# Kernel optimization log

Hardware: AMD Instinct MI355X
Metric: run time of the kernel (lower is better)

The kernel has to match this reference:

```python
import jax, jax.numpy as jnp
import numpy as np

N, E = 20000, 5000
IN_FT, OUT_FT = 128, 128
DENSITY = 0.01  # fraction of nonzeros in the incidence matrix


def setup_inputs() -> dict:
    key = jax.random.key(0)
    kx, kh, kw, kb = jax.random.split(key, 4)
    X = jax.random.normal(kx, (N, IN_FT), dtype=jnp.float32)
    H = (jax.random.uniform(kh, (N, E)) < DENSITY).astype(jnp.float32)
    # xavier_normal_ with gain=0.01
    xav_std = 0.01 * np.sqrt(2.0 / (IN_FT + OUT_FT))
    weight_trans = jax.random.normal(kw, (IN_FT, OUT_FT), dtype=jnp.float32) * xav_std
    bias = jax.random.normal(kb, (OUT_FT,), dtype=jnp.float32) * 0.01
    return {"X": X, "H": H, "weight_trans": weight_trans, "bias": bias}


def reference(X, H, weight_trans, bias):
    # X: [N, in_ft], H: [N, E] incidence
    Xw = X @ weight_trans                      # [N, out_ft]
    DV = jnp.sum(H, axis=1) + 1e-12            # node degrees, [N]
    DE = jnp.sum(H, axis=0) + 1e-12            # hyperedge degrees, [E]
    # G = diag(1/DV) @ H @ diag(1/DE) @ H^T applied to Xw, computed in the
    # efficient order without materializing the NxN matrix G:
    M = H.T @ Xw                               # [E, out_ft]
    M = M / DE[:, None]                        # diag(1/DE) scaling
    out = H @ M                                # [N, out_ft]
    out = out / DV[:, None]                    # diag(1/DV) scaling
    out = out + bias
    return jax.nn.relu(out)
```

## Files before the change

kernel.cpp:

```cpp
#include <hip/hip_runtime.h>
#include <hip/hip_bf16.h>

typedef unsigned long long u64;
typedef __attribute__((ext_vector_type(4))) float f32x4v;

#define N_NODES 20000
#define N_EDGES 5000
#define FT 128
#define NT 20
#define NRG 313
#define ROW_U64 80
#define COL_STRIDE 5120
#define MAX_DEG 320
#define MAX_NDEG 128

#define NTLOAD(p) __builtin_nontemporal_load((const f32x4v*)(p))

__global__ __launch_bounds__(256) void scan_fused(
    const float* __restrict__ H, u64* __restrict__ Hbt, u64* __restrict__ HbtT,
    const float2* __restrict__ X2, __hip_bfloat162* __restrict__ Xb2) {
  const int wid = threadIdx.x >> 6, lane = threadIdx.x & 63;

  if (blockIdx.x >= 1565) {
    for (int i = (blockIdx.x - 1565) * 256 + threadIdx.x; i < 1280000;
         i += 320 * 256)
      Xb2[i] = __float22bfloat162_rn(X2[i]);
    return;
  }

  const int gw = blockIdx.x * 4 + wid;
  const int t = gw % NT, rg = gw / NT;
  const int r0 = rg * 64;
  const int rows = min(64, N_NODES - r0);
  const int idx4 = t * 64 + lane;
  const bool lv = idx4 < 1250;

  u64 m0 = 0, m1 = 0, m2 = 0, m3 = 0;
  for (int kb = 0; kb < rows; kb += 8) {
    f32x4v vv[8];
#pragma unroll
    for (int k = 0; k < 8; ++k) vv[k] = (f32x4v){0.f, 0.f, 0.f, 0.f};
    if (lv) {
      const float* bp = H + (size_t)(r0 + kb) * N_EDGES + idx4 * 4;
#pragma unroll
      for (int k = 0; k < 8; ++k) vv[k] = NTLOAD(bp + (size_t)k * N_EDGES);
    }
#pragma unroll
    for (int k = 0; k < 8; ++k) {
      u64 b0 = __ballot(vv[k].x != 0.f);
      u64 b1 = __ballot(vv[k].y != 0.f);
      u64 b2 = __ballot(vv[k].z != 0.f);
      u64 b3 = __ballot(vv[k].w != 0.f);
      const bool keep = (lane == kb + k);
      m0 = keep ? b0 : m0;  m1 = keep ? b1 : m1;
      m2 = keep ? b2 : m2;  m3 = keep ? b3 : m3;
    }
  }
  if (lane < rows) {
    u64* hp = Hbt + (size_t)(r0 + lane) * ROW_U64 + t * 4;
    hp[0] = m0; hp[1] = m1; hp[2] = m2; hp[3] = m3;
  }
  u64 t0 = 0, t1 = 0, t2 = 0, t3 = 0;
  for (int l = 0; l < 64; ++l) {
    u64 c0 = __ballot((m0 >> l) & 1ull);
    u64 c1 = __ballot((m1 >> l) & 1ull);
    u64 c2 = __ballot((m2 >> l) & 1ull);
    u64 c3 = __ballot((m3 >> l) & 1ull);
    const bool keep = (lane == l);
    t0 = keep ? c0 : t0;  t1 = keep ? c1 : t1;
    t2 = keep ? c2 : t2;  t3 = keep ? c3 : t3;
  }
  u64* op = HbtT + (size_t)rg * COL_STRIDE + t * 256 + 4 * lane;
  op[0] = t0; op[1] = t1; op[2] = t2; op[3] = t3;
}

__global__ __launch_bounds__(256) void edge_gather(
    const __hip_bfloat162* __restrict__ Xb2,
    const u64* __restrict__ HbtT,
    float2* __restrict__ P2, int* __restrict__ de) {
  __shared__ int sidx[4][MAX_DEG];
  const int wid = threadIdx.x >> 6, lane = threadIdx.x & 63;
  const int e = blockIdx.x * 4 + wid;

  u64 cm[5];
#pragma unroll
  for (int q = 0; q < 5; ++q) {
    int u = q * 64 + lane;
    cm[q] = (u < NRG) ? HbtT[(size_t)u * COL_STRIDE + e] : 0ull;
  }
  int cnt = 0;
#pragma unroll
  for (int q = 0; q < 5; ++q) cnt += __popcll(cm[q]);
  int off = cnt;
  for (int d = 1; d < 64; d <<= 1) {
    int v = __shfl_up(off, d);
    if (lane >= d) off += v;
  }
  int total = __shfl(off, 63);
  off -= cnt;
#pragma unroll
  for (int q = 0; q < 5; ++q) {
    u64 w = cm[q];
    int rbase = q * 4096 + lane * 64;
    while (w) {
      int b = __ffsll(w) - 1;
      w &= w - 1;
      if (off < MAX_DEG) sidx[wid][off] = rbase + b;
      ++off;
    }
  }
  __builtin_amdgcn_s_waitcnt(0);
  int tt = min(total, MAX_DEG);

  float sx = 0.f, sy = 0.f;
  int g = 0;
  for (; g + 16 <= tt; g += 16) {
    int nn[16];
#pragma unroll
    for (int q = 0; q < 16; ++q) nn[q] = sidx[wid][g + q];
    float2 aa[16];
#pragma unroll
    for (int q = 0; q < 16; ++q) aa[q] = __bfloat1622float2(Xb2[nn[q] * 64 + lane]);
#pragma unroll
    for (int q = 0; q < 16; ++q) { sx += aa[q].x; sy += aa[q].y; }
  }
  for (; g < tt; ++g) {
    float2 a2 = __bfloat1622float2(Xb2[sidx[wid][g] * 64 + lane]);
    sx += a2.x; sy += a2.y;
  }
  P2[e * 64 + lane] = make_float2(sx, sy);
  if (lane == 0) de[e] = total;
}

__global__ __launch_bounds__(256) void gemm_M(
    const float* __restrict__ P, const float* __restrict__ W,
    const int* __restrict__ de, float* __restrict__ M) {
  int f = threadIdx.x & (FT - 1);
  int half = threadIdx.x >> 7;
  int base = blockIdx.x * 16 + half * 8;
#pragma unroll
  for (int g = 0; g < 8; g += 4) {
    int e = base + g;
    if (e >= N_EDGES) break;
    const float* p0 = P + (e + 0) * FT;
    const float* p1 = P + (e + 1) * FT;
    const float* p2 = P + (e + 2) * FT;
    const float* p3 = P + (e + 3) * FT;
    float a0 = 0.f, a1 = 0.f, a2 = 0.f, a3 = 0.f;
#pragma unroll 4
    for (int k = 0; k < FT; ++k) {
      float w = W[k * FT + f];
      a0 += p0[k] * w; a1 += p1[k] * w; a2 += p2[k] * w; a3 += p3[k] * w;
    }
    M[(e + 0) * FT + f] = a0 / ((float)de[e + 0] + 1e-12f);
    M[(e + 1) * FT + f] = a1 / ((float)de[e + 1] + 1e-12f);
    M[(e + 2) * FT + f] = a2 / ((float)de[e + 2] + 1e-12f);
    M[(e + 3) * FT + f] = a3 / ((float)de[e + 3] + 1e-12f);
  }
}

__global__ __launch_bounds__(256) void row_apply(
    const u64* __restrict__ Hbt,
    const float2* __restrict__ M2, const float2* __restrict__ bias2,
    float2* __restrict__ out2) {
  __shared__ int eidx[4][MAX_NDEG];
  const int wid = threadIdx.x >> 6, lane = threadIdx.x & 63;
  const int n = blockIdx.x * 4 + wid;
  const u64* hp = Hbt + (size_t)n * ROW_U64;
  u64 mlo = hp[lane];
  u64 mhi = (lane < ROW_U64 - 64) ? hp[64 + lane] : 0ull;
  int cnt = __popcll(mlo) + __popcll(mhi);
  int off = cnt;
  for (int d = 1; d < 64; d <<= 1) {
    int v = __shfl_up(off, d);
    if (lane >= d) off += v;
  }
  int total = __shfl(off, 63);
  off -= cnt;
  {
    int eb = (lane >> 2) * 256 + (lane & 3);
    u64 w = mlo;
    while (w) {
      int b = __ffsll(w) - 1; w &= w - 1;
      if (off < MAX_NDEG) eidx[wid][off] = eb + 4 * b;
      ++off;
    }
    int vp = 64 + lane;
    eb = (vp >> 2) * 256 + (vp & 3);
    w = mhi;
    while (w) {
      int b = __ffsll(w) - 1; w &= w - 1;
      if (off < MAX_NDEG) eidx[wid][off] = eb + 4 * b;
      ++off;
    }
  }
  __builtin_amdgcn_s_waitcnt(0);
  int tt = min(total, MAX_NDEG);

  float sx = 0.f, sy = 0.f;
  int g = 0;
  for (; g + 8 <= tt; g += 8) {
    int ee[8];
#pragma unroll
    for (int q = 0; q < 8; ++q) ee[q] = eidx[wid][g + q];
    float2 vv[8];
#pragma unroll
    for (int q = 0; q < 8; ++q) vv[q] = M2[(size_t)ee[q] * 64 + lane];
#pragma unroll
    for (int q = 0; q < 8; ++q) { sx += vv[q].x; sy += vv[q].y; }
  }
  for (; g < tt; ++g) {
    float2 v = M2[(size_t)eidx[wid][g] * 64 + lane];
    sx += v.x; sy += v.y;
  }
  float inv = 1.f / ((float)total + 1e-12f);
  float2 bb = bias2[lane];
  float2 o;
  o.x = fmaxf(fmaf(sx, inv, bb.x), 0.f);
  o.y = fmaxf(fmaf(sy, inv, bb.y), 0.f);
  out2[(size_t)n * 64 + lane] = o;
}

extern "C" void kernel_launch(void* const* d_in, const int* in_sizes, int n_in,
                              void* d_out, int out_size, void* d_ws, size_t ws_size,
                              hipStream_t stream) {
  const float* X    = (const float*)d_in[0];
  const float* H    = (const float*)d_in[1];
  const float* W    = (const float*)d_in[2];
  const float* bias = (const float*)d_in[3];
  float* out = (float*)d_out;

  int* ws = (int*)d_ws;
  u64* Hbt             = (u64*)ws;
  u64* HbtT            = (u64*)(ws + 3200000);
  __hip_bfloat162* Xb2 = (__hip_bfloat162*)(ws + 6476800);
  float* P             = (float*)(ws + 7756800);
  int* de              = ws + 8396800;
  float* M             = (float*)(ws + 8401920);

  scan_fused <<<1885, 256, 0, stream>>>(H, Hbt, HbtT, (const float2*)X, Xb2);
  edge_gather<<<1250, 256, 0, stream>>>(Xb2, HbtT, (float2*)P, de);
  gemm_M     <<<313, 256, 0, stream>>>(P, W, de, M);
  row_apply  <<<5000, 256, 0, stream>>>(Hbt, (const float2*)M,
                                        (const float2*)bias, (float2*)out);
}
```

Baseline: 613.8 us.

## Replace sparse gathers with dense bitmask-expanded MFMA GEMMs over the incidence matrix

Replaces the index-list gather kernels with three bf16 MFMA GEMMs. X@W is computed first, then H^T·Xw and H·M run as dense matmuls whose H operand is built on the fly by expanding bitmask bits into bf16 ones. Hbt is rewritten with interleaved bit packing so node rows map directly to MFMA fragments. This removes irregular gathers and per-wave index compaction, at the cost of doing dense work over a 1%-dense matrix and adding bf16 rounding on Xw and M.

```diff
diff --git a/kernel.cpp b/kernel.cpp
--- a/kernel.cpp
+++ b/kernel.cpp
@@ -2,7 +2,11 @@
 #include <hip/hip_bf16.h>
 
 typedef unsigned long long u64;
+typedef unsigned int u32;
+typedef unsigned short u16;
 typedef __attribute__((ext_vector_type(4))) float f32x4v;
+typedef __attribute__((ext_vector_type(16))) float f32x16;
+typedef __attribute__((ext_vector_type(8))) short bf16x8;
 
 #define N_NODES 20000
 #define N_EDGES 5000
@@ -11,20 +15,49 @@
 #define NRG 313
 #define ROW_U64 80
 #define COL_STRIDE 5120
-#define MAX_DEG 320
-#define MAX_NDEG 128
+#define XWT_S 20032
 
 #define NTLOAD(p) __builtin_nontemporal_load((const f32x4v*)(p))
+
+static __device__ __forceinline__ u64 spread4(u64 x) {
+  x = (x | (x << 24)) & 0x000000FF000000FFull;
+  x = (x | (x << 12)) & 0x000F000F000F000Full;
+  x = (x | (x << 6))  & 0x0303030303030303ull;
+  x = (x | (x << 3))  & 0x1111111111111111ull;
+  return x;
+}
+
+static __device__ __forceinline__ u16 f2bf(float x) {
+  u32 u = __float_as_uint(x);
+  u = (u + 0x7FFFu + ((u >> 16) & 1u)) >> 16;
+  return (u16)u;
+}
+
+static __device__ __forceinline__ bf16x8 expand8(u32 b) {
+  union { u32 u[4]; bf16x8 v; } r;
+  r.u[0] = (( b        & 1u) | ((( b >> 1) & 1u) << 16)) * 0x3F80u;
+  r.u[1] = (((b >> 2)  & 1u) | ((( b >> 3) & 1u) << 16)) * 0x3F80u;
+  r.u[2] = (((b >> 4)  & 1u) | ((( b >> 5) & 1u) << 16)) * 0x3F80u;
+  r.u[3] = (((b >> 6)  & 1u) | ((( b >> 7) & 1u) << 16)) * 0x3F80u;
+  return r.v;
+}
 
 __global__ __launch_bounds__(256) void scan_fused(
     const float* __restrict__ H, u64* __restrict__ Hbt, u64* __restrict__ HbtT,
-    const float2* __restrict__ X2, __hip_bfloat162* __restrict__ Xb2) {
+    const float2* __restrict__ X2, __hip_bfloat162* __restrict__ Xb2,
+    const float* __restrict__ Wf, u16* __restrict__ WtB) {
   const int wid = threadIdx.x >> 6, lane = threadIdx.x & 63;
 
   if (blockIdx.x >= 1565) {
     for (int i = (blockIdx.x - 1565) * 256 + threadIdx.x; i < 1280000;
          i += 320 * 256)
       Xb2[i] = __float22bfloat162_rn(X2[i]);
+    if (blockIdx.x == 1884) {
+      for (int i = threadIdx.x; i < FT * FT; i += 256) {
+        int f = i >> 7, k = i & 127;
+        WtB[i] = f2bf(Wf[k * FT + f]);
+      }
+    }
     return;
   }
 
@@ -58,7 +91,14 @@
   }
   if (lane < rows) {
     u64* hp = Hbt + (size_t)(r0 + lane) * ROW_U64 + t * 4;
-    hp[0] = m0; hp[1] = m1; hp[2] = m2; hp[3] = m3;
+#pragma unroll
+    for (int j = 0; j < 4; ++j) {
+      u64 p = spread4((m0 >> (16 * j)) & 0xFFFFull)
+            | (spread4((m1 >> (16 * j)) & 0xFFFFull) << 1)
+            | (spread4((m2 >> (16 * j)) & 0xFFFFull) << 2)
+            | (spread4((m3 >> (16 * j)) & 0xFFFFull) << 3);
+      hp[j] = p;
+    }
   }
   u64 t0 = 0, t1 = 0, t2 = 0, t3 = 0;
   for (int l = 0; l < 64; ++l) {
@@ -74,151 +114,107 @@
   op[0] = t0; op[1] = t1; op[2] = t2; op[3] = t3;
 }
 
-__global__ __launch_bounds__(256) void edge_gather(
-    const __hip_bfloat162* __restrict__ Xb2,
-    const u64* __restrict__ HbtT,
-    float2* __restrict__ P2, int* __restrict__ de) {
-  __shared__ int sidx[4][MAX_DEG];
-  const int wid = threadIdx.x >> 6, lane = threadIdx.x & 63;
-  const int e = blockIdx.x * 4 + wid;
-
-  u64 cm[5];
-#pragma unroll
-  for (int q = 0; q < 5; ++q) {
-    int u = q * 64 + lane;
-    cm[q] = (u < NRG) ? HbtT[(size_t)u * COL_STRIDE + e] : 0ull;
-  }
-  int cnt = 0;
-#pragma unroll
-  for (int q = 0; q < 5; ++q) cnt += __popcll(cm[q]);
-  int off = cnt;
-  for (int d = 1; d < 64; d <<= 1) {
-    int v = __shfl_up(off, d);
-    if (lane >= d) off += v;
-  }
-  int total = __shfl(off, 63);
-  off -= cnt;
-#pragma unroll
-  for (int q = 0; q < 5; ++q) {
-    u64 w = cm[q];
-    int rbase = q * 4096 + lane * 64;
-    while (w) {
-      int b = __ffsll(w) - 1;
-      w &= w - 1;
-      if (off < MAX_DEG) sidx[wid][off] = rbase + b;
-      ++off;
-    }
-  }
-  __builtin_amdgcn_s_waitcnt(0);
-  int tt = min(total, MAX_DEG);
-
-  float sx = 0.f, sy = 0.f;
-  int g = 0;
-  for (; g + 16 <= tt; g += 16) {
-    int nn[16];
-#pragma unroll
-    for (int q = 0; q < 16; ++q) nn[q] = sidx[wid][g + q];
-    float2 aa[16];
-#pragma unroll
-    for (int q = 0; q < 16; ++q) aa[q] = __bfloat1622float2(Xb2[nn[q] * 64 + lane]);
-#pragma unroll
-    for (int q = 0; q < 16; ++q) { sx += aa[q].x; sy += aa[q].y; }
-  }
-  for (; g < tt; ++g) {
-    float2 a2 = __bfloat1622float2(Xb2[sidx[wid][g] * 64 + lane]);
-    sx += a2.x; sy += a2.y;
-  }
-  P2[e * 64 + lane] = make_float2(sx, sy);
-  if (lane == 0) de[e] = total;
-}
-
-__global__ __launch_bounds__(256) void gemm_M(
-    const float* __restrict__ P, const float* __restrict__ W,
-    const int* __restrict__ de, float* __restrict__ M) {
-  int f = threadIdx.x & (FT - 1);
-  int half = threadIdx.x >> 7;
-  int base = blockIdx.x * 16 + half * 8;
-#pragma unroll
-  for (int g = 0; g < 8; g += 4) {
-    int e = base + g;
-    if (e >= N_EDGES) break;
-    const float* p0 = P + (e + 0) * FT;
-    const float* p1 = P + (e + 1) * FT;
-    const float* p2 = P + (e + 2) * FT;
-    const float* p3 = P + (e + 3) * FT;
-    float a0 = 0.f, a1 = 0.f, a2 = 0.f, a3 = 0.f;
-#pragma unroll 4
-    for (int k = 0; k < FT; ++k) {
-      float w = W[k * FT + f];
-      a0 += p0[k] * w; a1 += p1[k] * w; a2 += p2[k] * w; a3 += p3[k] * w;
-    }
-    M[(e + 0) * FT + f] = a0 / ((float)de[e + 0] + 1e-12f);
-    M[(e + 1) * FT + f] = a1 / ((float)de[e + 1] + 1e-12f);
-    M[(e + 2) * FT + f] = a2 / ((float)de[e + 2] + 1e-12f);
-    M[(e + 3) * FT + f] = a3 / ((float)de[e + 3] + 1e-12f);
-  }
-}
-
-__global__ __launch_bounds__(256) void row_apply(
-    const u64* __restrict__ Hbt,
-    const float2* __restrict__ M2, const float2* __restrict__ bias2,
-    float2* __restrict__ out2) {
-  __shared__ int eidx[4][MAX_NDEG];
-  const int wid = threadIdx.x >> 6, lane = threadIdx.x & 63;
-  const int n = blockIdx.x * 4 + wid;
-  const u64* hp = Hbt + (size_t)n * ROW_U64;
-  u64 mlo = hp[lane];
-  u64 mhi = (lane < ROW_U64 - 64) ? hp[64 + lane] : 0ull;
-  int cnt = __popcll(mlo) + __popcll(mhi);
-  int off = cnt;
-  for (int d = 1; d < 64; d <<= 1) {
-    int v = __shfl_up(off, d);
-    if (lane >= d) off += v;
-  }
-  int total = __shfl(off, 63);
-  off -= cnt;
+__global__ __launch_bounds__(256) void gemm_xw(
+    const u16* __restrict__ Xb, const u16* __restrict__ WtB,
+    u16* __restrict__ XwT) {
+  const int wave = threadIdx.x >> 6, lane = threadIdx.x & 63;
+  const int col = lane & 31, half = lane >> 5;
+  const int n0 = blockIdx.x * 32;
+  const int f0 = wave * 32;
+  if (n0 >= N_NODES) {
+    if (lane < 32)
+      for (int r = 0; r < 32; ++r)
+        XwT[(size_t)(f0 + r) * XWT_S + n0 + lane] = 0;
+    return;
+  }
+  f32x16 acc;
+#pragma unroll
+  for (int i = 0; i < 16; ++i) acc[i] = 0.f;
+  for (int k0 = 0; k0 < FT; k0 += 16) {
+    bf16x8 a = *(const bf16x8*)(WtB + (f0 + col) * FT + k0 + half * 8);
+    bf16x8 b = *(const bf16x8*)(Xb + (size_t)(n0 + col) * FT + k0 + half * 8);
+    acc = __builtin_amdgcn_mfma_f32_32x32x16_bf16(a, b, acc, 0, 0, 0);
+  }
+#pragma unroll
+  for (int r = 0; r < 16; ++r) {
+    int fr = (r & 3) + 8 * (r >> 2) + 4 * half;
+    XwT[(size_t)(f0 + fr) * XWT_S + n0 + col] = f2bf(acc[r]);
+  }
+}
+
+__global__ __launch_bounds__(256) void edge_gemm(
+    const u16* __restrict__ XwT, const u64* __restrict__ HbtT,
+    u16* __restrict__ MhT) {
+  const int wave = threadIdx.x >> 6, lane = threadIdx.x & 63;
+  const int col = lane & 31, half = lane >> 5;
+  const int et = blockIdx.x >> 1, fg = blockIdx.x & 1;
+  const int e0 = et * 64 + (wave >> 1) * 32;
+  const int f0 = fg * 64 + (wave & 1) * 32;
+
+  f32x16 acc;
+#pragma unroll
+  for (int i = 0; i < 16; ++i) acc[i] = 0.f;
+  float dv = 0.f;
+
+  for (int w = 0; w < NRG; ++w) {
+    u64 wd = HbtT[(size_t)w * COL_STRIDE + e0 + col];
+    dv += (float)__popcll(wd);
+    const u16* abase = XwT + (size_t)(f0 + col) * XWT_S + w * 64 + half * 8;
+#pragma unroll
+    for (int q = 0; q < 4; ++q) {
+      bf16x8 a = *(const bf16x8*)(abase + q * 16);
+      bf16x8 b = expand8((u32)(wd >> (q * 16 + half * 8)) & 0xFFu);
+      acc = __builtin_amdgcn_mfma_f32_32x32x16_bf16(a, b, acc, 0, 0, 0);
+    }
+  }
+  float inv = 1.f / (dv + 1e-12f);
+#pragma unroll
+  for (int r = 0; r < 16; ++r) {
+    int fr = f0 + (r & 3) + 8 * (r >> 2) + 4 * half;
+    MhT[(size_t)fr * COL_STRIDE + e0 + col] = f2bf(acc[r] * inv);
+  }
+}
+
+__global__ __launch_bounds__(256) void node_gemm(
+    const u64* __restrict__ Hbt, const u16* __restrict__ MhT,
+    const float* __restrict__ bias, float* __restrict__ out) {
+  __shared__ u64 ld[32][81];
+  const int tid = threadIdx.x;
+  const int wave = tid >> 6, lane = tid & 63;
+  const int col = lane & 31, half = lane >> 5;
+  const int n0 = blockIdx.x * 32;
   {
-    int eb = (lane >> 2) * 256 + (lane & 3);
-    u64 w = mlo;
-    while (w) {
-      int b = __ffsll(w) - 1; w &= w - 1;
-      if (off < MAX_NDEG) eidx[wid][off] = eb + 4 * b;
-      ++off;
-    }
-    int vp = 64 + lane;
-    eb = (vp >> 2) * 256 + (vp & 3);
-    w = mhi;
-    while (w) {
-      int b = __ffsll(w) - 1; w &= w - 1;
-      if (off < MAX_NDEG) eidx[wid][off] = eb + 4 * b;
-      ++off;
-    }
-  }
-  __builtin_amdgcn_s_waitcnt(0);
-  int tt = min(total, MAX_NDEG);
-
-  float sx = 0.f, sy = 0.f;
-  int g = 0;
-  for (; g + 8 <= tt; g += 8) {
-    int ee[8];
-#pragma unroll
-    for (int q = 0; q < 8; ++q) ee[q] = eidx[wid][g + q];
-    float2 vv[8];
-#pragma unroll
-    for (int q = 0; q < 8; ++q) vv[q] = M2[(size_t)ee[q] * 64 + lane];
-#pragma unroll
-    for (int q = 0; q < 8; ++q) { sx += vv[q].x; sy += vv[q].y; }
-  }
-  for (; g < tt; ++g) {
-    float2 v = M2[(size_t)eidx[wid][g] * 64 + lane];
-    sx += v.x; sy += v.y;
-  }
-  float inv = 1.f / ((float)total + 1e-12f);
-  float2 bb = bias2[lane];
-  float2 o;
-  o.x = fmaxf(fmaf(sx, inv, bb.x), 0.f);
-  o.y = fmaxf(fmaf(sy, inv, bb.y), 0.f);
-  out2[(size_t)n * 64 + lane] = o;
+    int r = tid & 31, g = tid >> 5;
+#pragma unroll
+    for (int i = 0; i < 10; ++i)
+      ld[r][g * 10 + i] = Hbt[(size_t)(n0 + r) * ROW_U64 + g * 10 + i];
+  }
+  __syncthreads();
+  const int f0 = wave * 32;
+  f32x16 acc;
+#pragma unroll
+  for (int i = 0; i < 16; ++i) acc[i] = 0.f;
+  float dv = 0.f;
+  for (int w = 0; w < ROW_U64; ++w) {
+    u64 word = ld[col][w];
+    if (half == 0) dv += (float)__popcll(word);
+    const u16* bbase = MhT + (size_t)(f0 + col) * COL_STRIDE + w * 64 + half * 8;
+#pragma unroll
+    for (int q = 0; q < 4; ++q) {
+      bf16x8 afrag = expand8((u32)(word >> (q * 16 + half * 8)) & 0xFFu);
+      bf16x8 bfrag = *(const bf16x8*)(bbase + q * 16);
+      acc = __builtin_amdgcn_mfma_f32_32x32x16_bf16(afrag, bfrag, acc, 0, 0, 0);
+    }
+  }
+  float inv = 1.f / (dv + 1e-12f);
+  float bb = bias[f0 + col];
+#pragma unroll
+  for (int r = 0; r < 16; ++r) {
+    int rr = (r & 3) + 8 * (r >> 2) + 4 * half;
+    float iv = __shfl(inv, rr);
+    float o = fmaxf(fmaf(acc[r], iv, bb), 0.f);
+    out[(size_t)(n0 + rr) * FT + f0 + col] = o;
+  }
 }
 
 extern "C" void kernel_launch(void* const* d_in, const int* in_sizes, int n_in,
@@ -233,14 +229,14 @@
   int* ws = (int*)d_ws;
   u64* Hbt             = (u64*)ws;
   u64* HbtT            = (u64*)(ws + 3200000);
-  __hip_bfloat162* Xb2 = (__hip_bfloat162*)(ws + 6476800);
-  float* P             = (float*)(ws + 7756800);
-  int* de              = ws + 8396800;
-  float* M             = (float*)(ws + 8401920);
-
-  scan_fused <<<1885, 256, 0, stream>>>(H, Hbt, HbtT, (const float2*)X, Xb2);
-  edge_gather<<<1250, 256, 0, stream>>>(Xb2, HbtT, (float2*)P, de);
-  gemm_M     <<<313, 256, 0, stream>>>(P, W, de, M);
-  row_apply  <<<5000, 256, 0, stream>>>(Hbt, (const float2*)M,
-                                        (const float2*)bias, (float2*)out);
-}
+  __hip_bfloat162* Xb2 = (__hip_bfloat162*)(ws + 6405120);
+  u16* MhT             = (u16*)(ws + 6405120);
+  u16* WtB             = (u16*)(ws + 7685120);
+  u16* XwT             = (u16*)(ws + 7693312);
+
+  scan_fused<<<1885, 256, 0, stream>>>(H, Hbt, HbtT, (const float2*)X, Xb2,
+                                       W, WtB);
+  gemm_xw   <<<626, 256, 0, stream>>>((const u16*)Xb2, WtB, XwT);
+  edge_gemm <<<160, 256, 0, stream>>>(XwT, HbtT, MhT);
+  node_gemm <<<625, 256, 0, stream>>>(Hbt, MhT, bias, out);
+}
```

Result: slower. 898.4 us (+46.4%).
